# Optimization experiments

Hardware: AMD Instinct MI355X
Metric: run time of the kernel (lower is better)

Reference implementation:

```python
import jax, jax.numpy as jnp
import numpy as np
import math

D_MODEL = 1024
N_HEADS = 16
D_HEAD = D_MODEL // N_HEADS
B, T = 2, 2048


def setup_inputs() -> dict:
    key = jax.random.key(0)
    ks = jax.random.split(key, 5)
    x = jax.random.normal(ks[0], (B, T, D_MODEL), dtype=jnp.float32)
    W_qkv = jax.random.normal(ks[1], (D_MODEL, 3 * D_MODEL), dtype=jnp.float32) * 0.02
    b_qkv = jnp.zeros((3 * D_MODEL,), dtype=jnp.float32)
    W_g = jax.random.normal(ks[2], (N_HEADS, D_HEAD, D_HEAD), dtype=jnp.float32) * 0.02
    W_out = jax.random.normal(ks[3], (D_MODEL, D_MODEL), dtype=jnp.float32) * 0.02
    b_out = jnp.zeros((D_MODEL,), dtype=jnp.float32)
    return {"x": x, "W_qkv": W_qkv, "b_qkv": b_qkv, "W_g": W_g, "W_out": W_out, "b_out": b_out}


def reference(x, W_qkv, b_qkv, W_g, W_out, b_out):
    b, t, d = x.shape
    h, dh = N_HEADS, D_HEAD
    qkv = x @ W_qkv + b_qkv                         # (B,T,3D)
    q, k, v = jnp.split(qkv, 3, axis=-1)
    # (B,T,D) -> (B,H,T,dh)
    q = q.reshape(b, t, h, dh).transpose(0, 2, 1, 3)
    k = k.reshape(b, t, h, dh).transpose(0, 2, 1, 3)
    v = v.reshape(b, t, h, dh).transpose(0, 2, 1, 3)
    scale = 1.0 / math.sqrt(dh)
    scores = jnp.einsum('bhtd,bhsd->bhts', q, k) * scale   # (B,H,T,T)
    causal = jnp.tril(jnp.ones((t, t), dtype=bool))
    scores = jnp.where(causal, scores, jnp.float32(-jnp.inf))
    attn = jax.nn.softmax(scores, axis=-1)
    # query-conditioned bilinear value gate (applied at each position)
    g = jax.nn.sigmoid(jnp.einsum('bhtd,hde->bhte', q, W_g))  # (B,H,T,dh)
    v = g * v
    out = jnp.einsum('bhts,bhsd->bhtd', attn, v)             # (B,H,T,dh)
    out = out.transpose(0, 2, 1, 3).reshape(b, t, d)
    return out @ W_out + b_out
```

## Files before the change

### kernel.cpp

```cpp
#include <hip/hip_runtime.h>
#include <hip/hip_bf16.h>

typedef unsigned short ushortT;
typedef __bf16 bf16x8 __attribute__((ext_vector_type(8)));
typedef __bf16 bf16x4 __attribute__((ext_vector_type(4)));
typedef float f32x4 __attribute__((ext_vector_type(4)));

#define T_SEQ 2048
#define DH 64
#define NH 16
#define DM 1024
#define TD 3072
#define BATCH 2
#define LOG2E 1.44269504f

__device__ inline ushortT f2bf(float f){
    union { float f; unsigned int u; } a; a.f = f;
    unsigned int r = a.u + 0x7fffu + ((a.u >> 16) & 1u);
    return (ushortT)(r >> 16);
}
__device__ inline float bf2f(ushortT u){
    union { float f; unsigned int u; } a; a.u = ((unsigned int)u) << 16;
    return a.f;
}

__device__ inline void gload_lds16(const void* g, void* l){
    __builtin_amdgcn_global_load_lds((const __attribute__((address_space(1))) void*)g,
                                     (__attribute__((address_space(3))) void*)l, 16, 0, 0);
}

__global__ __launch_bounds__(256) void cast_bf16_kernel(const float* __restrict__ in,
                                                        ushortT* __restrict__ out, int n){
    int i = (blockIdx.x * 256 + threadIdx.x) * 4;
    if (i < n){
        float4 v = *(const float4*)&in[i];
        out[i+0] = f2bf(v.x); out[i+1] = f2bf(v.y);
        out[i+2] = f2bf(v.z); out[i+3] = f2bf(v.w);
    }
}

__global__ __launch_bounds__(256) void transcast_kernel(const float* __restrict__ in,
                                                        ushortT* __restrict__ out, int K, int N){
    __shared__ float tile[64][65];
    int n0 = blockIdx.x * 64, k0 = blockIdx.y * 64;
    int tid = threadIdx.x;
    int c  = tid & 63;
    int r4 = tid >> 6;
#pragma unroll
    for (int i = 0; i < 16; i++){
        int k = r4 + i * 4;
        tile[k][c] = in[(size_t)(k0 + k) * N + n0 + c];
    }
    __syncthreads();
#pragma unroll
    for (int i = 0; i < 16; i++){
        int n = r4 + i * 4;
        out[(size_t)(n0 + n) * K + k0 + c] = f2bf(tile[c][n]);
    }
}

__global__ __launch_bounds__(256) void wg_transcast_kernel(const float* __restrict__ in,
                                                           ushortT* __restrict__ out){
    __shared__ float tile[64][65];
    int h = blockIdx.x;
    int tid = threadIdx.x;
    int c = tid & 63, r4 = tid >> 6;
#pragma unroll
    for (int i = 0; i < 16; i++){
        int d = r4 + i*4;
        tile[d][c] = in[h*4096 + d*64 + c];
    }
    __syncthreads();
#pragma unroll
    for (int i = 0; i < 16; i++){
        int e = r4 + i*4;
        out[h*4096 + e*64 + c] = f2bf(tile[c][e]);
    }
}

__device__ inline void store_out(ushortT* C, size_t i, float v){ C[i] = f2bf(v); }
__device__ inline void store_out(float*   C, size_t i, float v){ C[i] = v; }

template <typename OUT>
__global__ __launch_bounds__(256) void gemm_bf16_kernel(const ushortT* __restrict__ A,
                                                        const ushortT* __restrict__ BT,
                                                        const float* __restrict__ bias,
                                                        OUT* __restrict__ C,
                                                        int M, int N, int K){
    __shared__ __align__(16) ushortT As[2][128*32];
    __shared__ __align__(16) ushortT Bs[2][128*32];
    int tid = threadIdx.x;
    int m0 = blockIdx.x * 128;
    int n0 = blockIdx.y * 128;
    int wid = tid >> 6, lane = tid & 63;
    int l15 = lane & 15, g = lane >> 4;
    int wr = wid >> 1, wc = wid & 1;

    f32x4 acc[4][4];
#pragma unroll
    for (int i = 0; i < 4; i++)
#pragma unroll
        for (int j = 0; j < 4; j++) acc[i][j] = (f32x4){0.f,0.f,0.f,0.f};

    int srow = wid * 32 + (lane >> 2);
    int sch  = lane & 3;

#define GSTAGE(buf, k0)                                                                  \
    {                                                                                    \
        _Pragma("unroll")                                                                \
        for (int i_ = 0; i_ < 2; i_++){                                                  \
            int row_ = srow + i_ * 16;                                                   \
            const ushortT* asrc_ = A  + (size_t)(m0 + row_) * K + (k0) + sch * 8;        \
            const ushortT* bsrc_ = BT + (size_t)(n0 + row_) * K + (k0) + sch * 8;        \
            gload_lds16(asrc_, (char*)As[buf] + (wid*2 + i_) * 1024);                    \
            gload_lds16(bsrc_, (char*)Bs[buf] + (wid*2 + i_) * 1024);                    \
        }                                                                                \
    }

    GSTAGE(0, 0);
    __syncthreads();

    int nk = K >> 5;
    for (int kt = 0; kt < nk; kt++){
        int buf = kt & 1;
        if (kt + 1 < nk) GSTAGE(buf ^ 1, (kt + 1) * 32);

        bf16x8 af[4], bfr[4];
#pragma unroll
        for (int mi = 0; mi < 4; mi++){
            int r = wr*64 + mi*16 + l15;
            af[mi]  = *(const bf16x8*)(As[buf] + r*32 + g*8);
        }
#pragma unroll
        for (int ni = 0; ni < 4; ni++){
            int r = wc*64 + ni*16 + l15;
            bfr[ni] = *(const bf16x8*)(Bs[buf] + r*32 + g*8);
        }
#pragma unroll
        for (int mi = 0; mi < 4; mi++)
#pragma unroll
            for (int ni = 0; ni < 4; ni++)
                acc[mi][ni] = __builtin_amdgcn_mfma_f32_16x16x32_bf16(af[mi], bfr[ni], acc[mi][ni], 0, 0, 0);
        __syncthreads();
    }
#undef GSTAGE

#pragma unroll
    for (int mi = 0; mi < 4; mi++){
#pragma unroll
        for (int jj = 0; jj < 4; jj++){
            int mm = m0 + wr*64 + mi*16 + 4*g + jj;
#pragma unroll
            for (int ni = 0; ni < 4; ni++){
                int nn = n0 + wc*64 + ni*16 + l15;
                float v = acc[mi][ni][jj] + bias[nn];
                store_out(C, (size_t)mm * N + nn, v);
            }
        }
    }
}

__global__ __launch_bounds__(256) void gate_kernel(const ushortT* __restrict__ qkv,
                                                   const ushortT* __restrict__ WgT,
                                                   ushortT* __restrict__ vgT){
    __shared__ __align__(16) ushortT VT[64][72];
    int tblk = blockIdx.x, bh = blockIdx.y;
    int b = bh >> 4, h = bh & 15;
    int tid = threadIdx.x, wid = tid >> 6, lane = tid & 63;
    int l15 = lane & 15, g = lane >> 4;
    int t0 = tblk * 64;
    int tl = wid*16 + l15;

    const ushortT* qrow = qkv + ((size_t)b*T_SEQ + t0 + tl)*TD + h*DH;
    bf16x8 qf0 = *(const bf16x8*)(qrow + 8*g);
    bf16x8 qf1 = *(const bf16x8*)(qrow + 32 + 8*g);

    const ushortT* wbase = WgT + h*4096;
    const ushortT* vrow = qkv + ((size_t)b*T_SEQ + t0 + tl)*TD + 2*DM + h*DH;

#pragma unroll
    for (int ns = 0; ns < 4; ns++){
        int e = ns*16 + l15;
        bf16x8 wf0 = *(const bf16x8*)(wbase + e*64 + 8*g);
        bf16x8 wf1 = *(const bf16x8*)(wbase + e*64 + 32 + 8*g);
        f32x4 z = (f32x4){0.f,0.f,0.f,0.f};
        z = __builtin_amdgcn_mfma_f32_16x16x32_bf16(wf0, qf0, z, 0, 0, 0);
        z = __builtin_amdgcn_mfma_f32_16x16x32_bf16(wf1, qf1, z, 0, 0, 0);
        union { ushortT u[4]; uint2 v; } v4;
        v4.v = *(const uint2*)(vrow + ns*16 + 4*g);
#pragma unroll
        for (int jj = 0; jj < 4; jj++){
            float ex = __builtin_amdgcn_exp2f(-z[jj] * LOG2E);
            float gv = __builtin_amdgcn_rcpf(1.f + ex);
            VT[ns*16 + 4*g + jj][tl] = f2bf(gv * bf2f(v4.u[jj]));
        }
    }
    __syncthreads();
    for (int i = tid; i < 64*8; i += 256){
        int e = i >> 3, c8 = (i & 7) * 8;
        *(uint4*)&vgT[((size_t)bh * DH + e) * T_SEQ + t0 + c8] = *(const uint4*)&VT[e][c8];
    }
}

struct QState {
    bf16x8 qf0, qf1;
    float m_, lsum;
    f32x4 acc[4];
};

__device__ __forceinline__ void proc_tile(const ushortT* __restrict__ Kb,
                                          const ushortT* __restrict__ Vb,
                                          QState& S, bool diag,
                                          int wg, int l15, int g){
    int l7 = l15 & 7;
    f32x4 s[4];
    __builtin_amdgcn_s_setprio(1);
#pragma unroll
    for (int ns = 0; ns < 4; ns++){
        int kr = ns*16 + l15;
        bf16x8 kf0 = *(const bf16x8*)(Kb + kr*64 + ((g    ) ^ l7)*8);
        bf16x8 kf1 = *(const bf16x8*)(Kb + kr*64 + ((4 + g) ^ l7)*8);
        f32x4 z = (f32x4){0.f,0.f,0.f,0.f};
        z = __builtin_amdgcn_mfma_f32_16x16x32_bf16(kf0, S.qf0, z, 0, 0, 0);
        z = __builtin_amdgcn_mfma_f32_16x16x32_bf16(kf1, S.qf1, z, 0, 0, 0);
        s[ns] = z;
    }
    __builtin_amdgcn_s_setprio(0);

    float tmax = -INFINITY;
    if (diag){
        int qrel = wg*16 + l15;
#pragma unroll
        for (int ns = 0; ns < 4; ns++){
            int kbase = ((ns & 2) << 4) + 8*g + ((ns & 1) << 2);
#pragma unroll
            for (int jj = 0; jj < 4; jj++){
                if (kbase + jj > qrel) s[ns][jj] = -INFINITY;
                tmax = fmaxf(tmax, s[ns][jj]);
            }
        }
    } else {
#pragma unroll
        for (int ns = 0; ns < 4; ns++){
            float a = fmaxf(s[ns][0], s[ns][1]);
            float c = fmaxf(s[ns][2], s[ns][3]);
            tmax = fmaxf(tmax, fmaxf(a, c));
        }
    }
    tmax = fmaxf(tmax, __shfl_xor(tmax, 16, 64));
    tmax = fmaxf(tmax, __shfl_xor(tmax, 32, 64));

    float mnew = fmaxf(S.m_, tmax);
    float mc = mnew * LOG2E;
    float rs = 0.f;
    bf16x8 pa0, pa1;
#pragma unroll
    for (int jj = 0; jj < 4; jj++){
        float p0 = __builtin_amdgcn_exp2f(fmaf(s[0][jj], LOG2E, -mc));
        float p1 = __builtin_amdgcn_exp2f(fmaf(s[1][jj], LOG2E, -mc));
        float p2 = __builtin_amdgcn_exp2f(fmaf(s[2][jj], LOG2E, -mc));
        float p3 = __builtin_amdgcn_exp2f(fmaf(s[3][jj], LOG2E, -mc));
        rs += (p0 + p1) + (p2 + p3);
        pa0[jj]   = (__bf16)p0;
        pa0[4+jj] = (__bf16)p1;
        pa1[jj]   = (__bf16)p2;
        pa1[4+jj] = (__bf16)p3;
    }
    rs += __shfl_xor(rs, 16, 64);
    rs += __shfl_xor(rs, 32, 64);

    if (!__all(mnew == S.m_)){
        float alpha = __builtin_amdgcn_exp2f(fmaf(S.m_, LOG2E, -mc));
#pragma unroll
        for (int nt = 0; nt < 4; nt++)
#pragma unroll
            for (int jj = 0; jj < 4; jj++) S.acc[nt][jj] *= alpha;
        S.lsum *= alpha;
        S.m_ = mnew;
    }
    S.lsum += rs;

    __builtin_amdgcn_s_setprio(1);
#pragma unroll
    for (int ks = 0; ks < 2; ks++){
        bf16x8 pa = ks ? pa1 : pa0;
#pragma unroll
        for (int nt = 0; nt < 4; nt++){
            bf16x8 vf = *(const bf16x8*)(Vb + (nt*16 + l15)*64 + ((ks*4 + g) ^ l7)*8);
            S.acc[nt] = __builtin_amdgcn_mfma_f32_16x16x32_bf16(vf, pa, S.acc[nt], 0, 0, 0);
        }
    }
    __builtin_amdgcn_s_setprio(0);
}

__global__ __launch_bounds__(512) void attn_kernel(const ushortT* __restrict__ qkv,
                                                   const ushortT* __restrict__ vgT,
                                                   ushortT* __restrict__ obf){
    __shared__ __align__(16) ushortT Ks[2][64*64];
    __shared__ __align__(16) ushortT Vs[2][64*64];
    int id = blockIdx.x;
    int half = id >> 8, j = id & 255;
    int bh = (half << 4) | (j >> 4);
    int pp = j & 15;
    int pairid = half ? (15 - pp) : pp;
    int b = bh >> 4, h = bh & 15;
    int tid = threadIdx.x, wid = tid >> 6, lane = tid & 63;
    int l15 = lane & 15, g = lane >> 4;
    int grp = wid >> 2, wg = wid & 3;

    const ushortT* Kg = qkv + (size_t)b * T_SEQ * TD + DM + h * DH;
    const ushortT* Vg = vgT + (size_t)bh * DH * T_SEQ;

    int st_row = wid*8 + (lane >> 3);
    int st_c   = (lane & 7) ^ ((lane >> 3) & 7);
    int st_prow = (st_row & 0x20) | ((st_row & 0x0C) << 1) | ((st_row & 0x10) >> 2) | (st_row & 3);

#define STAGE_TILE(bufidx, kv0)                                                          \
    {                                                                                    \
        const ushortT* ksrc_ = Kg + (size_t)((kv0) + st_prow) * TD + st_c*8;             \
        const ushortT* vsrc_ = Vg + (size_t)st_row * T_SEQ + (kv0) + st_c*8;             \
        gload_lds16(ksrc_, (char*)Ks[bufidx] + wid*1024);                                \
        gload_lds16(vsrc_, (char*)Vs[bufidx] + wid*1024);                                \
    }

    int pA = pairid, pB = 31 - pairid;
    int myp = grp ? pB : pA;

    QState S;
    {
        int qrow = myp*64 + wg*16 + l15;
        const ushortT* qb = qkv + ((size_t)b * T_SEQ + qrow) * TD + h * DH;
        S.qf0 = *(const bf16x8*)(qb + 8*g);
        S.qf1 = *(const bf16x8*)(qb + 32 + 8*g);
    }
#pragma unroll
    for (int jq = 0; jq < 8; jq++){
        S.qf0[jq] = (__bf16)((float)S.qf0[jq] * 0.125f);
        S.qf1[jq] = (__bf16)((float)S.qf1[jq] * 0.125f);
    }
    S.m_ = -INFINITY; S.lsum = 0.f;
#pragma unroll
    for (int nt = 0; nt < 4; nt++) S.acc[nt] = (f32x4){0.f,0.f,0.f,0.f};

    STAGE_TILE(0, 0);
    __syncthreads();

    for (int t = 0; t <= pB; t++){
        int buf = t & 1;
        if (t < pB) STAGE_TILE(buf ^ 1, (t+1)*64);
        if (t <= myp)
            proc_tile(Ks[buf], Vs[buf], S, t == myp, wg, l15, g);
        __syncthreads();
    }
#undef STAGE_TILE

    float inv = 1.f / S.lsum;
    size_t orow = ((size_t)b * T_SEQ + myp*64 + wg*16 + l15) * DM + h*DH;
#pragma unroll
    for (int nt = 0; nt < 4; nt++){
        union { ushortT u[4]; uint2 v; } pk;
#pragma unroll
        for (int jj = 0; jj < 4; jj++) pk.u[jj] = f2bf(S.acc[nt][jj] * inv);
        *(uint2*)&obf[orow + nt*16 + 4*g] = pk.v;
    }
}

extern "C" void kernel_launch(void* const* d_in, const int* in_sizes, int n_in,
                              void* d_out, int out_size, void* d_ws, size_t ws_size,
                              hipStream_t stream){
    const float* x    = (const float*)d_in[0];
    const float* Wqkv = (const float*)d_in[1];
    const float* bqkv = (const float*)d_in[2];
    const float* Wg   = (const float*)d_in[3];
    const float* Wout = (const float*)d_in[4];
    const float* bout = (const float*)d_in[5];

    char* ws = (char*)d_ws;
    ushortT* xbf   = (ushortT*)(ws);
    ushortT* wqkvT = (ushortT*)(ws + 8388608);
    ushortT* woutT = (ushortT*)(ws + 14680064);
    ushortT* qkvb  = (ushortT*)(ws + 16777216);
    ushortT* vgT   = (ushortT*)(ws + 41943040);
    ushortT* obf   = (ushortT*)(ws + 50331648);
    ushortT* wgT   = (ushortT*)(ws + 58720256);

    cast_bf16_kernel<<<4096, 256, 0, stream>>>(x, xbf, 4194304);
    transcast_kernel<<<dim3(48,16), 256, 0, stream>>>(Wqkv, wqkvT, 1024, 3072);
    transcast_kernel<<<dim3(16,16), 256, 0, stream>>>(Wout, woutT, 1024, 1024);
    wg_transcast_kernel<<<16, 256, 0, stream>>>(Wg, wgT);
    gemm_bf16_kernel<ushortT><<<dim3(32,24), 256, 0, stream>>>(xbf, wqkvT, bqkv, qkvb, 4096, 3072, 1024);
    gate_kernel<<<dim3(32,32), 256, 0, stream>>>(qkvb, wgT, vgT);
    attn_kernel<<<512, 512, 0, stream>>>(qkvb, vgT, obf);
    gemm_bf16_kernel<float><<<dim3(32,8), 256, 0, stream>>>(obf, woutT, bout, (float*)d_out, 4096, 1024, 1024);
}
```

Before: 125.8 us.

## Process both paired query blocks per wave to reuse K/V fragments

The attention kernel now uses 4 waves per block instead of 8. Each wave holds two query states (one early and one late causal block) and computes both against each staged K/V tile, so K and V fragments read from LDS are shared between the two query blocks. The launch grid becomes 32x16 blocks of 256 threads with launch bounds allowing 2 blocks per CU, and each thread stages two rows per tile. The cost is higher register pressure from two accumulator states per wave and less wave-level parallelism inside each block.

```diff
diff --git a/kernel.cpp b/kernel.cpp
--- a/kernel.cpp
+++ b/kernel.cpp
@@ -202,34 +202,33 @@
     }
 }
 
-struct QState {
+struct QS {
     bf16x8 qf0, qf1;
     float m_, lsum;
     f32x4 acc[4];
 };
 
-__device__ __forceinline__ void proc_tile(const ushortT* __restrict__ Kb,
-                                          const ushortT* __restrict__ Vb,
-                                          QState& S, bool diag,
-                                          int wg, int l15, int g){
-    int l7 = l15 & 7;
-    f32x4 s[4];
-    __builtin_amdgcn_s_setprio(1);
-#pragma unroll
-    for (int ns = 0; ns < 4; ns++){
-        int kr = ns*16 + l15;
-        bf16x8 kf0 = *(const bf16x8*)(Kb + kr*64 + ((g    ) ^ l7)*8);
-        bf16x8 kf1 = *(const bf16x8*)(Kb + kr*64 + ((4 + g) ^ l7)*8);
-        f32x4 z = (f32x4){0.f,0.f,0.f,0.f};
-        z = __builtin_amdgcn_mfma_f32_16x16x32_bf16(kf0, S.qf0, z, 0, 0, 0);
-        z = __builtin_amdgcn_mfma_f32_16x16x32_bf16(kf1, S.qf1, z, 0, 0, 0);
-        s[ns] = z;
-    }
-    __builtin_amdgcn_s_setprio(0);
-
+__device__ __forceinline__ void qstate_init(QS& S, const ushortT* __restrict__ qkv,
+                                            int b, int qrow, int h, int g){
+    const ushortT* qb = qkv + ((size_t)b * T_SEQ + qrow) * TD + h * DH;
+    S.qf0 = *(const bf16x8*)(qb + 8*g);
+    S.qf1 = *(const bf16x8*)(qb + 32 + 8*g);
+#pragma unroll
+    for (int j = 0; j < 8; j++){
+        S.qf0[j] = (__bf16)((float)S.qf0[j] * 0.125f);
+        S.qf1[j] = (__bf16)((float)S.qf1[j] * 0.125f);
+    }
+    S.m_ = -INFINITY; S.lsum = 0.f;
+#pragma unroll
+    for (int nt = 0; nt < 4; nt++) S.acc[nt] = (f32x4){0.f,0.f,0.f,0.f};
+}
+
+__device__ __forceinline__ void softmax_state(f32x4* s, QS& S, bool diag,
+                                              int wid, int l15, int g,
+                                              bf16x8& pa0, bf16x8& pa1){
     float tmax = -INFINITY;
     if (diag){
-        int qrel = wg*16 + l15;
+        int qrel = wid*16 + l15;
 #pragma unroll
         for (int ns = 0; ns < 4; ns++){
             int kbase = ((ns & 2) << 4) + 8*g + ((ns & 1) << 2);
@@ -253,7 +252,6 @@
     float mnew = fmaxf(S.m_, tmax);
     float mc = mnew * LOG2E;
     float rs = 0.f;
-    bf16x8 pa0, pa1;
 #pragma unroll
     for (int jj = 0; jj < 4; jj++){
         float p0 = __builtin_amdgcn_exp2f(fmaf(s[0][jj], LOG2E, -mc));
@@ -279,68 +277,122 @@
         S.m_ = mnew;
     }
     S.lsum += rs;
-
+}
+
+__device__ __forceinline__ void proc_pair(const ushortT* __restrict__ Kb,
+                                          const ushortT* __restrict__ Vb,
+                                          QS& SA, QS& SB, bool aAct,
+                                          bool diagA, bool diagB,
+                                          int wid, int l15, int g){
+    int l7 = l15 & 7;
+    bf16x8 kf[8];
+#pragma unroll
+    for (int ns = 0; ns < 4; ns++){
+        int kr = ns*16 + l15;
+        kf[2*ns]   = *(const bf16x8*)(Kb + kr*64 + ((g    ) ^ l7)*8);
+        kf[2*ns+1] = *(const bf16x8*)(Kb + kr*64 + ((4 + g) ^ l7)*8);
+    }
+    f32x4 sA[4], sB[4];
     __builtin_amdgcn_s_setprio(1);
 #pragma unroll
-    for (int ks = 0; ks < 2; ks++){
-        bf16x8 pa = ks ? pa1 : pa0;
-#pragma unroll
-        for (int nt = 0; nt < 4; nt++){
-            bf16x8 vf = *(const bf16x8*)(Vb + (nt*16 + l15)*64 + ((ks*4 + g) ^ l7)*8);
-            S.acc[nt] = __builtin_amdgcn_mfma_f32_16x16x32_bf16(vf, pa, S.acc[nt], 0, 0, 0);
+    for (int ns = 0; ns < 4; ns++){
+        f32x4 z = (f32x4){0.f,0.f,0.f,0.f};
+        z = __builtin_amdgcn_mfma_f32_16x16x32_bf16(kf[2*ns],   SB.qf0, z, 0, 0, 0);
+        z = __builtin_amdgcn_mfma_f32_16x16x32_bf16(kf[2*ns+1], SB.qf1, z, 0, 0, 0);
+        sB[ns] = z;
+    }
+    if (aAct){
+#pragma unroll
+        for (int ns = 0; ns < 4; ns++){
+            f32x4 z = (f32x4){0.f,0.f,0.f,0.f};
+            z = __builtin_amdgcn_mfma_f32_16x16x32_bf16(kf[2*ns],   SA.qf0, z, 0, 0, 0);
+            z = __builtin_amdgcn_mfma_f32_16x16x32_bf16(kf[2*ns+1], SA.qf1, z, 0, 0, 0);
+            sA[ns] = z;
         }
     }
     __builtin_amdgcn_s_setprio(0);
-}
-
-__global__ __launch_bounds__(512) void attn_kernel(const ushortT* __restrict__ qkv,
-                                                   const ushortT* __restrict__ vgT,
-                                                   ushortT* __restrict__ obf){
+
+    bf16x8 paA0, paA1, paB0, paB1;
+    softmax_state(sB, SB, diagB, wid, l15, g, paB0, paB1);
+    if (aAct) softmax_state(sA, SA, diagA, wid, l15, g, paA0, paA1);
+
+    __builtin_amdgcn_s_setprio(1);
+    if (aAct){
+#pragma unroll
+        for (int ks = 0; ks < 2; ks++){
+            bf16x8 pB_ = ks ? paB1 : paB0;
+            bf16x8 pA_ = ks ? paA1 : paA0;
+#pragma unroll
+            for (int nt = 0; nt < 4; nt++){
+                bf16x8 vf = *(const bf16x8*)(Vb + (nt*16 + l15)*64 + ((ks*4 + g) ^ l7)*8);
+                SB.acc[nt] = __builtin_amdgcn_mfma_f32_16x16x32_bf16(vf, pB_, SB.acc[nt], 0, 0, 0);
+                SA.acc[nt] = __builtin_amdgcn_mfma_f32_16x16x32_bf16(vf, pA_, SA.acc[nt], 0, 0, 0);
+            }
+        }
+    } else {
+#pragma unroll
+        for (int ks = 0; ks < 2; ks++){
+            bf16x8 pB_ = ks ? paB1 : paB0;
+#pragma unroll
+            for (int nt = 0; nt < 4; nt++){
+                bf16x8 vf = *(const bf16x8*)(Vb + (nt*16 + l15)*64 + ((ks*4 + g) ^ l7)*8);
+                SB.acc[nt] = __builtin_amdgcn_mfma_f32_16x16x32_bf16(vf, pB_, SB.acc[nt], 0, 0, 0);
+            }
+        }
+    }
+    __builtin_amdgcn_s_setprio(0);
+}
+
+__device__ __forceinline__ void write_state(QS& S, ushortT* __restrict__ obf,
+                                            int b, int qblk, int h,
+                                            int wid, int l15, int g){
+    float inv = 1.f / S.lsum;
+    size_t orow = ((size_t)b * T_SEQ + qblk*64 + wid*16 + l15) * DM + h*DH;
+#pragma unroll
+    for (int nt = 0; nt < 4; nt++){
+        union { ushortT u[4]; uint2 v; } pk;
+#pragma unroll
+        for (int jj = 0; jj < 4; jj++) pk.u[jj] = f2bf(S.acc[nt][jj] * inv);
+        *(uint2*)&obf[orow + nt*16 + 4*g] = pk.v;
+    }
+}
+
+__global__ __launch_bounds__(256, 2) void attn_kernel(const ushortT* __restrict__ qkv,
+                                                      const ushortT* __restrict__ vgT,
+                                                      ushortT* __restrict__ obf){
     __shared__ __align__(16) ushortT Ks[2][64*64];
     __shared__ __align__(16) ushortT Vs[2][64*64];
-    int id = blockIdx.x;
-    int half = id >> 8, j = id & 255;
-    int bh = (half << 4) | (j >> 4);
-    int pp = j & 15;
-    int pairid = half ? (15 - pp) : pp;
+    int bh = blockIdx.x, y = blockIdx.y;
+    int pairid = (y < 8) ? y : 23 - y;
     int b = bh >> 4, h = bh & 15;
     int tid = threadIdx.x, wid = tid >> 6, lane = tid & 63;
     int l15 = lane & 15, g = lane >> 4;
-    int grp = wid >> 2, wg = wid & 3;
 
     const ushortT* Kg = qkv + (size_t)b * T_SEQ * TD + DM + h * DH;
     const ushortT* Vg = vgT + (size_t)bh * DH * T_SEQ;
 
-    int st_row = wid*8 + (lane >> 3);
-    int st_c   = (lane & 7) ^ ((lane >> 3) & 7);
-    int st_prow = (st_row & 0x20) | ((st_row & 0x0C) << 1) | ((st_row & 0x10) >> 2) | (st_row & 3);
+    int st_row0 = wid*8 + (lane >> 3);
+    int st_c    = (lane & 7) ^ ((lane >> 3) & 7);
 
 #define STAGE_TILE(bufidx, kv0)                                                          \
     {                                                                                    \
-        const ushortT* ksrc_ = Kg + (size_t)((kv0) + st_prow) * TD + st_c*8;             \
-        const ushortT* vsrc_ = Vg + (size_t)st_row * T_SEQ + (kv0) + st_c*8;             \
-        gload_lds16(ksrc_, (char*)Ks[bufidx] + wid*1024);                                \
-        gload_lds16(vsrc_, (char*)Vs[bufidx] + wid*1024);                                \
+        _Pragma("unroll")                                                                \
+        for (int i_ = 0; i_ < 2; i_++){                                                  \
+            int row_  = st_row0 + i_*32;                                                 \
+            int prow_ = (row_ & 0x20) | ((row_ & 0x0C) << 1) |                           \
+                        ((row_ & 0x10) >> 2) | (row_ & 3);                               \
+            const ushortT* ksrc_ = Kg + (size_t)((kv0) + prow_) * TD + st_c*8;           \
+            const ushortT* vsrc_ = Vg + (size_t)row_ * T_SEQ + (kv0) + st_c*8;           \
+            gload_lds16(ksrc_, (char*)Ks[bufidx] + wid*1024 + i_*4096);                  \
+            gload_lds16(vsrc_, (char*)Vs[bufidx] + wid*1024 + i_*4096);                  \
+        }                                                                                \
     }
 
     int pA = pairid, pB = 31 - pairid;
-    int myp = grp ? pB : pA;
-
-    QState S;
-    {
-        int qrow = myp*64 + wg*16 + l15;
-        const ushortT* qb = qkv + ((size_t)b * T_SEQ + qrow) * TD + h * DH;
-        S.qf0 = *(const bf16x8*)(qb + 8*g);
-        S.qf1 = *(const bf16x8*)(qb + 32 + 8*g);
-    }
-#pragma unroll
-    for (int jq = 0; jq < 8; jq++){
-        S.qf0[jq] = (__bf16)((float)S.qf0[jq] * 0.125f);
-        S.qf1[jq] = (__bf16)((float)S.qf1[jq] * 0.125f);
-    }
-    S.m_ = -INFINITY; S.lsum = 0.f;
-#pragma unroll
-    for (int nt = 0; nt < 4; nt++) S.acc[nt] = (f32x4){0.f,0.f,0.f,0.f};
+
+    QS SA, SB;
+    qstate_init(SA, qkv, b, pA*64 + wid*16 + l15, h, g);
+    qstate_init(SB, qkv, b, pB*64 + wid*16 + l15, h, g);
 
     STAGE_TILE(0, 0);
     __syncthreads();
@@ -348,21 +400,13 @@
     for (int t = 0; t <= pB; t++){
         int buf = t & 1;
         if (t < pB) STAGE_TILE(buf ^ 1, (t+1)*64);
-        if (t <= myp)
-            proc_tile(Ks[buf], Vs[buf], S, t == myp, wg, l15, g);
+        proc_pair(Ks[buf], Vs[buf], SA, SB, t <= pA, t == pA, t == pB, wid, l15, g);
         __syncthreads();
     }
 #undef STAGE_TILE
 
-    float inv = 1.f / S.lsum;
-    size_t orow = ((size_t)b * T_SEQ + myp*64 + wg*16 + l15) * DM + h*DH;
-#pragma unroll
-    for (int nt = 0; nt < 4; nt++){
-        union { ushortT u[4]; uint2 v; } pk;
-#pragma unroll
-        for (int jj = 0; jj < 4; jj++) pk.u[jj] = f2bf(S.acc[nt][jj] * inv);
-        *(uint2*)&obf[orow + nt*16 + 4*g] = pk.v;
-    }
+    write_state(SA, obf, b, pA, h, wid, l15, g);
+    write_state(SB, obf, b, pB, h, wid, l15, g);
 }
 
 extern "C" void kernel_launch(void* const* d_in, const int* in_sizes, int n_in,
@@ -390,6 +434,6 @@
     wg_transcast_kernel<<<16, 256, 0, stream>>>(Wg, wgT);
     gemm_bf16_kernel<ushortT><<<dim3(32,24), 256, 0, stream>>>(xbf, wqkvT, bqkv, qkvb, 4096, 3072, 1024);
     gate_kernel<<<dim3(32,32), 256, 0, stream>>>(qkvb, wgT, vgT);
-    attn_kernel<<<512, 512, 0, stream>>>(qkvb, vgT, obf);
+    attn_kernel<<<dim3(32,16), 256, 0, stream>>>(qkvb, vgT, obf);
     gemm_bf16_kernel<float><<<dim3(32,8), 256, 0, stream>>>(obf, woutT, bout, (float*)d_out, 4096, 1024, 1024);
 }
```

Result: no change. 125.9 us (+0.1%).

## Drop LDS staging in attention; load K/V tiles directly from global per wave

Applied to the files above, without the earlier changes.

The attention kernel no longer stages K and V tiles into double-buffered shared memory with block-wide barriers. Each wave now reads its K and V MFMA fragments straight from global memory (relying on L2/L1). The grid changes from 512 blocks of 512 threads, each pairing a short and a long query block, to 1024 blocks of 256 threads, each handling one query block in a serpentine order. This removes LDS traffic and syncs but loses reuse across waves, so every wave issues redundant global loads, and the load balancing from pairing is replaced by relying on block scheduling.

```diff
diff --git a/kernel.cpp b/kernel.cpp
--- a/kernel.cpp
+++ b/kernel.cpp
@@ -202,34 +202,18 @@
     }
 }
 
-struct QState {
+struct QS {
     bf16x8 qf0, qf1;
     float m_, lsum;
     f32x4 acc[4];
 };
 
-__device__ __forceinline__ void proc_tile(const ushortT* __restrict__ Kb,
-                                          const ushortT* __restrict__ Vb,
-                                          QState& S, bool diag,
-                                          int wg, int l15, int g){
-    int l7 = l15 & 7;
-    f32x4 s[4];
-    __builtin_amdgcn_s_setprio(1);
-#pragma unroll
-    for (int ns = 0; ns < 4; ns++){
-        int kr = ns*16 + l15;
-        bf16x8 kf0 = *(const bf16x8*)(Kb + kr*64 + ((g    ) ^ l7)*8);
-        bf16x8 kf1 = *(const bf16x8*)(Kb + kr*64 + ((4 + g) ^ l7)*8);
-        f32x4 z = (f32x4){0.f,0.f,0.f,0.f};
-        z = __builtin_amdgcn_mfma_f32_16x16x32_bf16(kf0, S.qf0, z, 0, 0, 0);
-        z = __builtin_amdgcn_mfma_f32_16x16x32_bf16(kf1, S.qf1, z, 0, 0, 0);
-        s[ns] = z;
-    }
-    __builtin_amdgcn_s_setprio(0);
-
+__device__ __forceinline__ void softmax_state(f32x4* s, QS& S, bool diag,
+                                              int wid, int l15, int g,
+                                              bf16x8& pa0, bf16x8& pa1){
     float tmax = -INFINITY;
     if (diag){
-        int qrel = wg*16 + l15;
+        int qrel = wid*16 + l15;
 #pragma unroll
         for (int ns = 0; ns < 4; ns++){
             int kbase = ((ns & 2) << 4) + 8*g + ((ns & 1) << 2);
@@ -253,7 +237,6 @@
     float mnew = fmaxf(S.m_, tmax);
     float mc = mnew * LOG2E;
     float rs = 0.f;
-    bf16x8 pa0, pa1;
 #pragma unroll
     for (int jj = 0; jj < 4; jj++){
         float p0 = __builtin_amdgcn_exp2f(fmaf(s[0][jj], LOG2E, -mc));
@@ -279,83 +262,91 @@
         S.m_ = mnew;
     }
     S.lsum += rs;
-
-    __builtin_amdgcn_s_setprio(1);
-#pragma unroll
-    for (int ks = 0; ks < 2; ks++){
-        bf16x8 pa = ks ? pa1 : pa0;
-#pragma unroll
-        for (int nt = 0; nt < 4; nt++){
-            bf16x8 vf = *(const bf16x8*)(Vb + (nt*16 + l15)*64 + ((ks*4 + g) ^ l7)*8);
-            S.acc[nt] = __builtin_amdgcn_mfma_f32_16x16x32_bf16(vf, pa, S.acc[nt], 0, 0, 0);
-        }
-    }
-    __builtin_amdgcn_s_setprio(0);
-}
-
-__global__ __launch_bounds__(512) void attn_kernel(const ushortT* __restrict__ qkv,
-                                                   const ushortT* __restrict__ vgT,
-                                                   ushortT* __restrict__ obf){
-    __shared__ __align__(16) ushortT Ks[2][64*64];
-    __shared__ __align__(16) ushortT Vs[2][64*64];
+}
+
+__global__ __launch_bounds__(256, 4) void attn_kernel(const ushortT* __restrict__ qkv,
+                                                      const ushortT* __restrict__ vgT,
+                                                      ushortT* __restrict__ obf){
     int id = blockIdx.x;
-    int half = id >> 8, j = id & 255;
-    int bh = (half << 4) | (j >> 4);
-    int pp = j & 15;
-    int pairid = half ? (15 - pp) : pp;
+    int bh = id & 31;
+    int y  = id >> 5;
+    int ya = y & 7, yb = y >> 3;
+    int qblk = yb*8 + ((yb & 1) ? 7 - ya : ya);
     int b = bh >> 4, h = bh & 15;
     int tid = threadIdx.x, wid = tid >> 6, lane = tid & 63;
     int l15 = lane & 15, g = lane >> 4;
-    int grp = wid >> 2, wg = wid & 3;
-
-    const ushortT* Kg = qkv + (size_t)b * T_SEQ * TD + DM + h * DH;
-    const ushortT* Vg = vgT + (size_t)bh * DH * T_SEQ;
-
-    int st_row = wid*8 + (lane >> 3);
-    int st_c   = (lane & 7) ^ ((lane >> 3) & 7);
-    int st_prow = (st_row & 0x20) | ((st_row & 0x0C) << 1) | ((st_row & 0x10) >> 2) | (st_row & 3);
-
-#define STAGE_TILE(bufidx, kv0)                                                          \
-    {                                                                                    \
-        const ushortT* ksrc_ = Kg + (size_t)((kv0) + st_prow) * TD + st_c*8;             \
-        const ushortT* vsrc_ = Vg + (size_t)st_row * T_SEQ + (kv0) + st_c*8;             \
-        gload_lds16(ksrc_, (char*)Ks[bufidx] + wid*1024);                                \
-        gload_lds16(vsrc_, (char*)Vs[bufidx] + wid*1024);                                \
-    }
-
-    int pA = pairid, pB = 31 - pairid;
-    int myp = grp ? pB : pA;
-
-    QState S;
+    int l7 = l15 & 7;
+
+    QS S;
     {
-        int qrow = myp*64 + wg*16 + l15;
+        int qrow = qblk*64 + wid*16 + l15;
         const ushortT* qb = qkv + ((size_t)b * T_SEQ + qrow) * TD + h * DH;
         S.qf0 = *(const bf16x8*)(qb + 8*g);
         S.qf1 = *(const bf16x8*)(qb + 32 + 8*g);
-    }
-#pragma unroll
-    for (int jq = 0; jq < 8; jq++){
-        S.qf0[jq] = (__bf16)((float)S.qf0[jq] * 0.125f);
-        S.qf1[jq] = (__bf16)((float)S.qf1[jq] * 0.125f);
-    }
-    S.m_ = -INFINITY; S.lsum = 0.f;
-#pragma unroll
-    for (int nt = 0; nt < 4; nt++) S.acc[nt] = (f32x4){0.f,0.f,0.f,0.f};
-
-    STAGE_TILE(0, 0);
-    __syncthreads();
-
-    for (int t = 0; t <= pB; t++){
-        int buf = t & 1;
-        if (t < pB) STAGE_TILE(buf ^ 1, (t+1)*64);
-        if (t <= myp)
-            proc_tile(Ks[buf], Vs[buf], S, t == myp, wg, l15, g);
-        __syncthreads();
-    }
-#undef STAGE_TILE
+#pragma unroll
+        for (int j = 0; j < 8; j++){
+            S.qf0[j] = (__bf16)((float)S.qf0[j] * 0.125f);
+            S.qf1[j] = (__bf16)((float)S.qf1[j] * 0.125f);
+        }
+        S.m_ = -INFINITY; S.lsum = 0.f;
+#pragma unroll
+        for (int nt = 0; nt < 4; nt++) S.acc[nt] = (f32x4){0.f,0.f,0.f,0.f};
+    }
+
+    const ushortT* kp = qkv + (size_t)b * T_SEQ * TD + DM + h * DH;
+    const ushortT* vp = vgT + (size_t)bh * DH * T_SEQ;
+    int koff[8];
+#pragma unroll
+    for (int ns = 0; ns < 4; ns++){
+        int r  = ns*16 + l15;
+        int pr = (r & 0x20) | ((r & 0x0C) << 1) | ((r & 0x10) >> 2) | (r & 3);
+        koff[2*ns]   = pr*TD + 8*g;
+        koff[2*ns+1] = pr*TD + 32 + 8*g;
+    }
+    int voff[2][4];
+#pragma unroll
+    for (int ks = 0; ks < 2; ks++)
+#pragma unroll
+        for (int nt = 0; nt < 4; nt++)
+            voff[ks][nt] = (nt*16 + l15)*T_SEQ + (ks*4 + g)*8;
+
+    for (int t = 0; t <= qblk; t++){
+        bf16x8 kf[8];
+#pragma unroll
+        for (int i = 0; i < 8; i++) kf[i] = *(const bf16x8*)(kp + koff[i]);
+
+        f32x4 s[4];
+        __builtin_amdgcn_s_setprio(1);
+#pragma unroll
+        for (int ns = 0; ns < 4; ns++){
+            f32x4 z = (f32x4){0.f,0.f,0.f,0.f};
+            z = __builtin_amdgcn_mfma_f32_16x16x32_bf16(kf[2*ns],   S.qf0, z, 0, 0, 0);
+            z = __builtin_amdgcn_mfma_f32_16x16x32_bf16(kf[2*ns+1], S.qf1, z, 0, 0, 0);
+            s[ns] = z;
+        }
+        __builtin_amdgcn_s_setprio(0);
+
+        bf16x8 pa0, pa1;
+        softmax_state(s, S, t == qblk, wid, l15, g, pa0, pa1);
+
+        __builtin_amdgcn_s_setprio(1);
+#pragma unroll
+        for (int ks = 0; ks < 2; ks++){
+            bf16x8 pa = ks ? pa1 : pa0;
+#pragma unroll
+            for (int nt = 0; nt < 4; nt++){
+                bf16x8 vf = *(const bf16x8*)(vp + voff[ks][nt]);
+                S.acc[nt] = __builtin_amdgcn_mfma_f32_16x16x32_bf16(vf, pa, S.acc[nt], 0, 0, 0);
+            }
+        }
+        __builtin_amdgcn_s_setprio(0);
+
+        kp += 64 * TD;
+        vp += 64;
+    }
 
     float inv = 1.f / S.lsum;
-    size_t orow = ((size_t)b * T_SEQ + myp*64 + wg*16 + l15) * DM + h*DH;
+    size_t orow = ((size_t)b * T_SEQ + qblk*64 + wid*16 + l15) * DM + h*DH;
 #pragma unroll
     for (int nt = 0; nt < 4; nt++){
         union { ushortT u[4]; uint2 v; } pk;
@@ -390,6 +381,6 @@
     wg_transcast_kernel<<<16, 256, 0, stream>>>(Wg, wgT);
     gemm_bf16_kernel<ushortT><<<dim3(32,24), 256, 0, stream>>>(xbf, wqkvT, bqkv, qkvb, 4096, 3072, 1024);
     gate_kernel<<<dim3(32,32), 256, 0, stream>>>(qkvb, wgT, vgT);
-    attn_kernel<<<512, 512, 0, stream>>>(qkvb, vgT, obf);
+    attn_kernel<<<1024, 256, 0, stream>>>(qkvb, vgT, obf);
     gemm_bf16_kernel<float><<<dim3(32,8), 256, 0, stream>>>(obf, woutT, bout, (float*)d_out, 4096, 1024, 1024);
 }
```

Result: slower. 206.2 us (+63.9%).
